# Kernel tuning notes

Measured on AMD Instinct MI355X. Metric: run time of the kernel, lower is better.

The kernel has to match this reference:

```python
import jax, jax.numpy as jnp
import numpy as np

N = 50000      # nodes
E = 800000     # edges (before self loops)
IN = 256       # in_dim
HID = 64       # hidden_dim
H = 4          # heads
OUT = 32       # out_dim (latent); conv2 out_channels = 2*OUT
NEG_SLOPE = 0.2
EPS = 1e-5


def setup_inputs() -> dict:
    key = jax.random.key(0)
    ks = jax.random.split(key, 12)
    s = 0.05
    x = jax.random.normal(ks[0], (N, IN), dtype=jnp.float32)
    edge_index = jax.random.randint(ks[1], (2, E), 0, N, dtype=jnp.int64)
    # conv1: GATv2Conv(IN -> HID, heads=H, concat=True)
    W1l = jax.random.normal(ks[2], (IN, H * HID), dtype=jnp.float32) * s
    W1r = jax.random.normal(ks[3], (IN, H * HID), dtype=jnp.float32) * s
    att1 = jax.random.normal(ks[4], (H, HID), dtype=jnp.float32) * s
    b1 = jnp.zeros((H * HID,), dtype=jnp.float32)
    # BatchNorm1 (affine)
    g1 = jnp.ones((H * HID,), dtype=jnp.float32) + 0.1 * jax.random.normal(ks[5], (H * HID,), dtype=jnp.float32)
    be1 = 0.1 * jax.random.normal(ks[6], (H * HID,), dtype=jnp.float32)
    # conv2: GATv2Conv(H*HID -> 2*OUT, heads=H, concat=False)
    W2l = jax.random.normal(ks[7], (H * HID, H * 2 * OUT), dtype=jnp.float32) * s
    W2r = jax.random.normal(ks[8], (H * HID, H * 2 * OUT), dtype=jnp.float32) * s
    att2 = jax.random.normal(ks[9], (H, 2 * OUT), dtype=jnp.float32) * s
    b2 = jnp.zeros((2 * OUT,), dtype=jnp.float32)
    return {"x": x, "edge_index": edge_index, "W1l": W1l, "W1r": W1r,
            "att1": att1, "b1": b1, "g1": g1, "be1": be1,
            "W2l": W2l, "W2r": W2r, "att2": att2, "b2": b2}


def _gatv2(x, Wl, Wr, att, bias, src, dst, heads, ch, concat):
    # PyG GATv2Conv: xl = lin_l(x) (source side), xr = lin_r(x) (target side)
    xl = (x @ Wl).reshape(N, heads, ch)
    xr = (x @ Wr).reshape(N, heads, ch)
    e = jax.nn.leaky_relu(xl[src] + xr[dst], NEG_SLOPE)      # [E', H, C]
    score = jnp.einsum('ehc,hc->eh', e, att)                 # [E', H]
    # segment softmax over edges grouped by destination node
    m = jax.ops.segment_max(score, dst, num_segments=N)
    ex = jnp.exp(score - m[dst])
    den = jax.ops.segment_sum(ex, dst, num_segments=N)
    alpha = ex / den[dst]                                    # [E', H]
    out = jax.ops.segment_sum(alpha[..., None] * xl[src], dst, num_segments=N)  # [N, H, C]
    out = out.reshape(N, heads * ch) if concat else out.mean(axis=1)
    return out + bias


def _bn(x, gamma, beta):
    mu = x.mean(axis=0)
    var = x.var(axis=0)  # biased, as in nn.BatchNorm1d training mode
    xh = (x - mu) / jnp.sqrt(var + EPS)
    if gamma is None:
        return xh
    return xh * gamma + beta


def reference(x, edge_index, W1l, W1r, att1, b1, g1, be1, W2l, W2r, att2, b2):
    loops = jnp.arange(N, dtype=edge_index.dtype)
    src = jnp.concatenate([edge_index[0], loops])
    dst = jnp.concatenate([edge_index[1], loops])
    h = _gatv2(x, W1l, W1r, att1, b1, src, dst, H, HID, True)   # [N, H*HID]
    h = jax.nn.relu(_bn(h, g1, be1))
    o = _gatv2(h, W2l, W2r, att2, b2, src, dst, H, 2 * OUT, False)  # [N, 2*OUT]
    z_mu = _bn(o[:, :OUT], None, None)          # BatchNorm(affine=False)
    z_sig = jax.nn.sigmoid(o[:, OUT:])
    return (z_mu, z_sig)
```

## Files before the change

### kernel.cpp

```cpp
#include <hip/hip_runtime.h>
#include <math.h>

#define EPSBN 1e-5f

typedef __attribute__((ext_vector_type(8))) short short8;
typedef __attribute__((ext_vector_type(8))) _Float16 f16x8;
typedef __attribute__((ext_vector_type(2))) _Float16 h2;
typedef __attribute__((ext_vector_type(4))) float f32x4;

#if defined(__has_builtin)
#if __has_builtin(__builtin_amdgcn_fdot2)
#define HAVE_FDOT2 1
#endif
#endif

__device__ __forceinline__ unsigned short f2h(float f) {
  _Float16 h = (_Float16)f;
  return __builtin_bit_cast(unsigned short, h);
}
__device__ __forceinline__ h2 bch(unsigned u) { return __builtin_bit_cast(h2, u); }
__device__ __forceinline__ unsigned h2u(h2 v) { return __builtin_bit_cast(unsigned, v); }
__device__ __forceinline__ int swz(int b) { return b ^ (((b >> 7) & 3) << 4); }

__global__ __launch_bounds__(256) void gemm_dual(const unsigned short* __restrict__ Ab,
                                                 const unsigned short* __restrict__ Wt,
                                                 unsigned short* __restrict__ C, int M) {
  __shared__ __align__(16) short As[4096];
  __shared__ __align__(16) short Bs[4096];
  const int tid = threadIdx.x;
  const int lane = tid & 63, w = tid >> 6;
  const int wr = w >> 1, wc = w & 1;
  const int bm = blockIdx.x * 128, bn = blockIdx.y * 128;

  const int srow = tid >> 2;
  const int scol = (tid & 3) << 4;
  const char* gA = (const char*)Ab + (size_t)(bm + srow) * 512 + scol;
  const char* gB = (const char*)Wt + (size_t)(bn + srow) * 512 + scol;
  char* wA0 = (char*)As + swz(tid * 16);
  char* wA1 = (char*)As + swz((256 + tid) * 16);
  char* wB0 = (char*)Bs + swz(tid * 16);
  char* wB1 = (char*)Bs + swz((256 + tid) * 16);

  int aoff[4], boff[4];
#pragma unroll
  for (int i = 0; i < 4; ++i) {
    aoff[i] = swz(((wr * 64 + i * 16 + (lane & 15)) << 6) + ((lane >> 4) << 4));
    boff[i] = swz(((wc * 64 + i * 16 + (lane & 15)) << 6) + ((lane >> 4) << 4));
  }

  f32x4 acc[4][4] = {};
  short8 ra0 = *(const short8*)(gA);
  short8 ra1 = *(const short8*)(gA + 64 * 512);
  short8 rb0 = *(const short8*)(gB);
  short8 rb1 = *(const short8*)(gB + 64 * 512);

  for (int ks = 0; ks < 8; ++ks) {
    *(short8*)wA0 = ra0; *(short8*)wA1 = ra1;
    *(short8*)wB0 = rb0; *(short8*)wB1 = rb1;
    __syncthreads();
    if (ks < 7) {
      int off = (ks + 1) * 64;
      ra0 = *(const short8*)(gA + off);
      ra1 = *(const short8*)(gA + 64 * 512 + off);
      rb0 = *(const short8*)(gB + off);
      rb1 = *(const short8*)(gB + 64 * 512 + off);
    }
    short8 af[4], bfr[4];
#pragma unroll
    for (int i = 0; i < 4; ++i) af[i] = *(const short8*)((const char*)As + aoff[i]);
#pragma unroll
    for (int i = 0; i < 4; ++i) bfr[i] = *(const short8*)((const char*)Bs + boff[i]);
#pragma unroll
    for (int mr = 0; mr < 4; ++mr)
#pragma unroll
      for (int nc = 0; nc < 4; ++nc)
        acc[mr][nc] = __builtin_amdgcn_mfma_f32_16x16x32_f16(
            __builtin_bit_cast(f16x8, bfr[nc]), __builtin_bit_cast(f16x8, af[mr]),
            acc[mr][nc], 0, 0, 0);
    __syncthreads();
  }

#pragma unroll
  for (int mr = 0; mr < 4; ++mr) {
    int row = bm + wr * 64 + mr * 16 + (lane & 15);
    if (row < M) {
#pragma unroll
      for (int nc = 0; nc < 4; ++nc) {
        int col = bn + wc * 64 + nc * 16 + ((lane >> 4) << 2);
        ushort4 o;
        o.x = f2h(acc[mr][nc][0]); o.y = f2h(acc[mr][nc][1]);
        o.z = f2h(acc[mr][nc][2]); o.w = f2h(acc[mr][nc][3]);
        *(ushort4*)&C[(size_t)row * 512 + col] = o;
      }
    }
  }
}

__global__ void prep(const float* __restrict__ x, const float* __restrict__ W1l,
                     const float* __restrict__ W1r, const float* __restrict__ W2l,
                     const float* __restrict__ W2r, const int* __restrict__ ei,
                     unsigned short* __restrict__ xh, unsigned short* __restrict__ Wt1,
                     unsigned short* __restrict__ Wt2, int* __restrict__ cnt,
                     int n4x, int Etot, int E) {
  int t = blockIdx.x * 256 + threadIdx.x;
  if (t < n4x) {
    float4 v = *(const float4*)&x[(size_t)t * 4];
    ushort4 o;
    o.x = f2h(v.x); o.y = f2h(v.y); o.z = f2h(v.z); o.w = f2h(v.w);
    *(ushort4*)&xh[(size_t)t * 4] = o;
    return;
  }
  t -= n4x;
  if (t < 131072) {
    int n = t >> 8, k = t & 255;
    const float* W = (n < 256) ? W1l : W1r;
    Wt1[t] = f2h(W[k * 256 + (n & 255)]);
    return;
  }
  t -= 131072;
  if (t < 131072) {
    int n = t >> 8, k = t & 255;
    const float* W = (n < 256) ? W2l : W2r;
    Wt2[t] = f2h(W[k * 256 + (n & 255)]);
    return;
  }
  t -= 131072;
  if (t < Etot) {
    int d = (t < E) ? ei[E + t] : t - E;
    atomicAdd(&cnt[d], 1);
  }
}

__global__ __launch_bounds__(1024) void scan_block(const int* __restrict__ cnt,
                                                   int* __restrict__ rowptr,
                                                   int N, int Etot) {
  __shared__ int lds[1024];
  int t = threadIdx.x;
  int strip = (N + 1023) >> 10;
  int lo = t * strip, hi = min(lo + strip, N);
  int s = 0;
  for (int i = lo; i < hi && lo < N; ++i) s += cnt[i];
  lds[t] = s;
  __syncthreads();
  for (int off = 1; off < 1024; off <<= 1) {
    int v = (t >= off) ? lds[t - off] : 0;
    __syncthreads();
    lds[t] += v;
    __syncthreads();
  }
  int base = lds[t] - s;
  for (int i = lo; i < hi && lo < N; ++i) { rowptr[i] = base; base += cnt[i]; }
  if (t == 1023) rowptr[N] = Etot;
}

__global__ void scatter_src(const int* __restrict__ ei, const int* __restrict__ rowptr,
                            int* __restrict__ cur, int* __restrict__ srcs,
                            int Etot, int E) {
  int e = blockIdx.x * 256 + threadIdx.x;
  if (e >= Etot) return;
  int s, d;
  if (e < E) { s = ei[e]; d = ei[E + e]; } else { s = e - E; d = s; }
  int pos = rowptr[d] + atomicAdd(&cur[d], 1);
  srcs[pos] = s;
}

template <int CONCAT>
__global__ __launch_bounds__(256) void gat_fused(const unsigned short* __restrict__ xlr,
                                                 const float* __restrict__ att,
                                                 const float* __restrict__ bias,
                                                 const int* __restrict__ rowptr,
                                                 const int* __restrict__ srcs,
                                                 void* __restrict__ outv, int N) {
  int d = (blockIdx.x << 2) + (threadIdx.x >> 6);
  if (d >= N) return;
  int lane = threadIdx.x & 63;
  uint2 ub = *(const uint2*)&xlr[(size_t)d * 512 + 256 + lane * 4];
  h2 xb01 = bch(ub.x), xb23 = bch(ub.y);
  float4 wf = *(const float4*)&att[lane * 4];
  h2 w06a = {(_Float16)(0.6f * wf.x), (_Float16)(0.6f * wf.y)};
  h2 w06b = {(_Float16)(0.6f * wf.z), (_Float16)(0.6f * wf.w)};
  h2 w04a = {(_Float16)(0.4f * wf.x), (_Float16)(0.4f * wf.y)};
  h2 w04b = {(_Float16)(0.4f * wf.z), (_Float16)(0.4f * wf.w)};
  int i0 = rowptr[d], end = rowptr[d + 1];
  int eM1 = end - 1;
  float den = 0.f, a0 = 0.f, a1 = 0.f, a2 = 0.f, a3 = 0.f;

  auto GLD = [&](int j) -> uint2 {
    int jj = min(j, eM1);
    return *(const uint2*)&xlr[(size_t)srcs[jj] * 512 + lane * 4];
  };
  auto PROC = [&](uint2 cur) {
    h2 c01 = bch(cur.x), c23 = bch(cur.y);
    h2 e01 = c01 + xb01, e23 = c23 + xb23;
    float p;
#ifdef HAVE_FDOT2
    h2 ab01 = bch(h2u(e01) & 0x7FFF7FFFu);
    h2 ab23 = bch(h2u(e23) & 0x7FFF7FFFu);
    p = __builtin_amdgcn_fdot2(ab01, w04a,
        __builtin_amdgcn_fdot2(ab23, w04b,
        __builtin_amdgcn_fdot2(e01, w06a,
        __builtin_amdgcn_fdot2(e23, w06b, 0.f, false), false), false), false);
#else
    {
      float e0 = (float)e01.x, e1 = (float)e01.y, e2 = (float)e23.x, e3 = (float)e23.y;
      float l0 = fmaxf(e0, 0.2f * e0), l1 = fmaxf(e1, 0.2f * e1);
      float l2 = fmaxf(e2, 0.2f * e2), l3 = fmaxf(e3, 0.2f * e3);
      p = l0 * wf.x + l1 * wf.y + l2 * wf.z + l3 * wf.w;
    }
#endif
    p += __shfl_xor(p, 1);
    p += __shfl_xor(p, 2);
    p += __shfl_xor(p, 4);
    p += __shfl_xor(p, 8);
    float ex = __expf(p);
    den += ex;
    a0 = fmaf(ex, (float)c01.x, a0);
    a1 = fmaf(ex, (float)c01.y, a1);
    a2 = fmaf(ex, (float)c23.x, a2);
    a3 = fmaf(ex, (float)c23.y, a3);
  };

  uint2 b0 = GLD(i0), b1 = GLD(i0 + 1), b2 = GLD(i0 + 2), b3 = GLD(i0 + 3);
  for (int i = i0; i < end; i += 4) {
    uint2 c0 = b0, c1 = b1, c2 = b2, c3 = b3;
    b0 = GLD(i + 4); b1 = GLD(i + 5); b2 = GLD(i + 6); b3 = GLD(i + 7);
    PROC(c0);
    if (i + 1 < end) PROC(c1);
    if (i + 2 < end) PROC(c2);
    if (i + 3 < end) PROC(c3);
  }

  float inv = 1.f / den;
  if (CONCAT) {
    float4 bb = *(const float4*)&bias[lane * 4];
    ushort4 o;
    o.x = f2h(a0 * inv + bb.x); o.y = f2h(a1 * inv + bb.y);
    o.z = f2h(a2 * inv + bb.z); o.w = f2h(a3 * inv + bb.w);
    *(ushort4*)&((unsigned short*)outv)[(size_t)d * 256 + lane * 4] = o;
  } else {
    float v0 = a0 * inv, v1 = a1 * inv, v2 = a2 * inv, v3 = a3 * inv;
    v0 += __shfl_xor(v0, 16); v0 += __shfl_xor(v0, 32);
    v1 += __shfl_xor(v1, 16); v1 += __shfl_xor(v1, 32);
    v2 += __shfl_xor(v2, 16); v2 += __shfl_xor(v2, 32);
    v3 += __shfl_xor(v3, 16); v3 += __shfl_xor(v3, 32);
    if (lane < 16) {
      float4 bb = *(const float4*)&bias[lane * 4];
      *(float4*)&((float*)outv)[(size_t)d * 64 + lane * 4] =
          make_float4(0.25f * v0 + bb.x, 0.25f * v1 + bb.y,
                      0.25f * v2 + bb.z, 0.25f * v3 + bb.w);
    }
  }
}

__global__ __launch_bounds__(256) void bn_stats(const unsigned short* __restrict__ h,
                                                float* __restrict__ sums, int N) {
  __shared__ float4 rs[4][64], rq[4][64];
  int lane = threadIdx.x & 63;
  int rg = threadIdx.x >> 6;
  int c4 = lane * 4;
  float s0 = 0, s1 = 0, s2 = 0, s3 = 0, q0 = 0, q1 = 0, q2 = 0, q3 = 0;
  for (int r = blockIdx.x * 4 + rg; r < N; r += gridDim.x * 4) {
    uint2 v = *(const uint2*)&h[(size_t)r * 256 + c4];
    h2 a = bch(v.x), b = bch(v.y);
    float f0 = (float)a.x, f1 = (float)a.y, f2 = (float)b.x, f3 = (float)b.y;
    s0 += f0; q0 += f0 * f0;
    s1 += f1; q1 += f1 * f1;
    s2 += f2; q2 += f2 * f2;
    s3 += f3; q3 += f3 * f3;
  }
  rs[rg][lane] = make_float4(s0, s1, s2, s3);
  rq[rg][lane] = make_float4(q0, q1, q2, q3);
  __syncthreads();
  if (rg == 0) {
    float4 S = rs[0][lane], Q = rq[0][lane];
#pragma unroll
    for (int g = 1; g < 4; ++g) {
      float4 t = rs[g][lane]; S.x += t.x; S.y += t.y; S.z += t.z; S.w += t.w;
      float4 u = rq[g][lane]; Q.x += u.x; Q.y += u.y; Q.z += u.z; Q.w += u.w;
    }
    atomicAdd(&sums[c4 + 0], S.x); atomicAdd(&sums[c4 + 1], S.y);
    atomicAdd(&sums[c4 + 2], S.z); atomicAdd(&sums[c4 + 3], S.w);
    atomicAdd(&sums[256 + c4 + 0], Q.x); atomicAdd(&sums[256 + c4 + 1], Q.y);
    atomicAdd(&sums[256 + c4 + 2], Q.z); atomicAdd(&sums[256 + c4 + 3], Q.w);
  }
}

__global__ void bn_coef(const float* __restrict__ sums, const float* __restrict__ g,
                        const float* __restrict__ be, float* __restrict__ coef, int N) {
  int c = threadIdx.x;
  float inv_n = 1.f / (float)N;
  float mu = sums[c] * inv_n;
  float var = sums[256 + c] * inv_n - mu * mu;
  float sc = g[c] * rsqrtf(var + EPSBN);
  coef[c] = sc;
  coef[256 + c] = be[c] - mu * sc;
}

__global__ void bn_apply_relu(unsigned short* __restrict__ h, const float* __restrict__ coef,
                              int N) {
  int i = blockIdx.x * 256 + threadIdx.x;
  if (i >= N * 32) return;
  int base = i * 8, c = base & 255;
  uint4 v = *(const uint4*)&h[base];
  h2 p0 = bch(v.x), p1 = bch(v.y), p2 = bch(v.z), p3 = bch(v.w);
  float4 sA = *(const float4*)&coef[c];
  float4 sB = *(const float4*)&coef[c + 4];
  float4 hA = *(const float4*)&coef[256 + c];
  float4 hB = *(const float4*)&coef[256 + c + 4];
  float r0 = fmaf((float)p0.x, sA.x, hA.x); r0 = r0 > 0.f ? r0 : 0.f;
  float r1 = fmaf((float)p0.y, sA.y, hA.y); r1 = r1 > 0.f ? r1 : 0.f;
  float r2 = fmaf((float)p1.x, sA.z, hA.z); r2 = r2 > 0.f ? r2 : 0.f;
  float r3 = fmaf((float)p1.y, sA.w, hA.w); r3 = r3 > 0.f ? r3 : 0.f;
  float r4 = fmaf((float)p2.x, sB.x, hB.x); r4 = r4 > 0.f ? r4 : 0.f;
  float r5 = fmaf((float)p2.y, sB.y, hB.y); r5 = r5 > 0.f ? r5 : 0.f;
  float r6 = fmaf((float)p3.x, sB.z, hB.z); r6 = r6 > 0.f ? r6 : 0.f;
  float r7 = fmaf((float)p3.y, sB.w, hB.w); r7 = r7 > 0.f ? r7 : 0.f;
  uint4 o;
  o.x = (unsigned)f2h(r0) | ((unsigned)f2h(r1) << 16);
  o.y = (unsigned)f2h(r2) | ((unsigned)f2h(r3) << 16);
  o.z = (unsigned)f2h(r4) | ((unsigned)f2h(r5) << 16);
  o.w = (unsigned)f2h(r6) | ((unsigned)f2h(r7) << 16);
  *(uint4*)&h[base] = o;
}

__global__ __launch_bounds__(256) void bn2_stats(const float* __restrict__ o,
                                                 float* __restrict__ sums, int N) {
  __shared__ float4 lsum[256], lqum[256];
  int t = threadIdx.x;
  int q = t & 7, rs = t >> 3;
  float4 S = {0, 0, 0, 0}, Q = {0, 0, 0, 0};
  for (int r = blockIdx.x * 32 + rs; r < N; r += gridDim.x * 32) {
    float4 v = *(const float4*)&o[(size_t)r * 64 + q * 4];
    S.x += v.x; Q.x += v.x * v.x;
    S.y += v.y; Q.y += v.y * v.y;
    S.z += v.z; Q.z += v.z * v.z;
    S.w += v.w; Q.w += v.w * v.w;
  }
  lsum[t] = S; lqum[t] = Q;
  __syncthreads();
  if (t < 8) {
    float4 Sa = lsum[t], Qa = lqum[t];
    for (int k = 1; k < 32; ++k) {
      float4 a = lsum[t + 8 * k], b = lqum[t + 8 * k];
      Sa.x += a.x; Sa.y += a.y; Sa.z += a.z; Sa.w += a.w;
      Qa.x += b.x; Qa.y += b.y; Qa.z += b.z; Qa.w += b.w;
    }
    atomicAdd(&sums[t * 4 + 0], Sa.x); atomicAdd(&sums[t * 4 + 1], Sa.y);
    atomicAdd(&sums[t * 4 + 2], Sa.z); atomicAdd(&sums[t * 4 + 3], Sa.w);
    atomicAdd(&sums[32 + t * 4 + 0], Qa.x); atomicAdd(&sums[32 + t * 4 + 1], Qa.y);
    atomicAdd(&sums[32 + t * 4 + 2], Qa.z); atomicAdd(&sums[32 + t * 4 + 3], Qa.w);
  }
}

__global__ void write_out(const float* __restrict__ o, const float* __restrict__ sums,
                          float* __restrict__ out, int N) {
  int t = threadIdx.x;
  int n = blockIdx.x * 4 + (t >> 6);
  if (n >= N) return;
  int lane = t & 63;
  float v = o[(size_t)n * 64 + lane];
  if (lane < 32) {
    float inv_n = 1.f / (float)N;
    float mu = sums[lane] * inv_n;
    float var = sums[32 + lane] * inv_n - mu * mu;
    out[(size_t)n * 32 + lane] = (v - mu) * rsqrtf(var + EPSBN);
  } else {
    out[(size_t)N * 32 + (size_t)n * 32 + (lane - 32)] = 1.f / (1.f + __expf(-v));
  }
}

extern "C" void kernel_launch(void* const* d_in, const int* in_sizes, int n_in,
                              void* d_out, int out_size, void* d_ws, size_t ws_size,
                              hipStream_t stream) {
  const float* x    = (const float*)d_in[0];
  const int*   ei   = (const int*)d_in[1];
  const float* W1l  = (const float*)d_in[2];
  const float* W1r  = (const float*)d_in[3];
  const float* att1 = (const float*)d_in[4];
  const float* b1   = (const float*)d_in[5];
  const float* g1   = (const float*)d_in[6];
  const float* be1  = (const float*)d_in[7];
  const float* W2l  = (const float*)d_in[8];
  const float* W2r  = (const float*)d_in[9];
  const float* att2 = (const float*)d_in[10];
  const float* b2   = (const float*)d_in[11];
  float* out = (float*)d_out;

  const int N = in_sizes[0] / 256;
  const int E = in_sizes[1] / 2;
  const int Etot = E + N;
  const int Npad = ((N + 127) / 128) * 128;

  char* ws = (char*)d_ws;
  unsigned short* xh  = (unsigned short*)ws; ws += (size_t)Npad * 256 * 2;
  unsigned short* hb  = (unsigned short*)ws; ws += (size_t)Npad * 256 * 2;
  unsigned short* AB  = (unsigned short*)ws; ws += (size_t)Npad * 512 * 2;
  unsigned short* Wt1 = (unsigned short*)ws; ws += (size_t)512 * 256 * 2;
  unsigned short* Wt2 = (unsigned short*)ws; ws += (size_t)512 * 256 * 2;
  float* o    = (float*)ws;  ws += (size_t)N * 64 * 4;
  int* rowptr = (int*)ws;    ws += (size_t)(N + 1) * 4;
  int* cnt    = (int*)ws;    ws += (size_t)N * 4;
  int* srcs   = (int*)ws;    ws += (size_t)Etot * 4;
  float* sums1 = (float*)ws; ws += 512 * 4;
  float* sums2 = (float*)ws; ws += 64 * 4;
  float* coef1 = (float*)ws; ws += 512 * 4;

  dim3 gemmGrid(Npad / 128, 4);
  int dstBlocks = (N + 3) / 4;
  int n4x = N * 64;
  int prepTotal = n4x + 131072 + 131072 + Etot;

  hipMemsetAsync(cnt, 0, (size_t)N * 4, stream);
  hipMemsetAsync(sums1, 0, 512 * 4, stream);
  hipMemsetAsync(sums2, 0, 64 * 4, stream);
  prep<<<(prepTotal + 255) / 256, 256, 0, stream>>>(x, W1l, W1r, W2l, W2r, ei,
                                                    xh, Wt1, Wt2, cnt, n4x, Etot, E);
  scan_block<<<1, 1024, 0, stream>>>(cnt, rowptr, N, Etot);
  hipMemsetAsync(cnt, 0, (size_t)N * 4, stream);
  scatter_src<<<(Etot + 255) / 256, 256, 0, stream>>>(ei, rowptr, cnt, srcs, Etot, E);

  gemm_dual<<<gemmGrid, 256, 0, stream>>>(xh, Wt1, AB, N);
  gat_fused<1><<<dstBlocks, 256, 0, stream>>>(AB, att1, b1, rowptr, srcs, hb, N);
  bn_stats<<<512, 256, 0, stream>>>(hb, sums1, N);
  bn_coef<<<1, 256, 0, stream>>>(sums1, g1, be1, coef1, N);
  bn_apply_relu<<<(N * 32 + 255) / 256, 256, 0, stream>>>(hb, coef1, N);

  gemm_dual<<<gemmGrid, 256, 0, stream>>>(hb, Wt2, AB, N);
  gat_fused<0><<<dstBlocks, 256, 0, stream>>>(AB, att2, b2, rowptr, srcs, o, N);
  bn2_stats<<<128, 256, 0, stream>>>(o, sums2, N);
  write_out<<<dstBlocks, 256, 0, stream>>>(o, sums2, out, N);
}
```

Measured before the change: 610.4 us.

## Replace single-block CSR scan with three-phase multi-block scan

```diff
diff --git a/kernel.cpp b/kernel.cpp
--- a/kernel.cpp
+++ b/kernel.cpp
@@ -131,26 +131,76 @@
   }
 }
 
-__global__ __launch_bounds__(1024) void scan_block(const int* __restrict__ cnt,
-                                                   int* __restrict__ rowptr,
-                                                   int N, int Etot) {
-  __shared__ int lds[1024];
+__global__ __launch_bounds__(256) void scan_partial(const int* __restrict__ cnt,
+                                                    int* __restrict__ bsum, int N) {
+  __shared__ int red[256];
   int t = threadIdx.x;
-  int strip = (N + 1023) >> 10;
-  int lo = t * strip, hi = min(lo + strip, N);
+  int i = blockIdx.x * 1024 + t * 4;
   int s = 0;
-  for (int i = lo; i < hi && lo < N; ++i) s += cnt[i];
-  lds[t] = s;
+  if (i + 3 < N) {
+    int4 v = *(const int4*)&cnt[i];
+    s = v.x + v.y + v.z + v.w;
+  } else {
+    for (int k = 0; k < 4; ++k)
+      if (i + k < N) s += cnt[i + k];
+  }
+  red[t] = s;
   __syncthreads();
-  for (int off = 1; off < 1024; off <<= 1) {
-    int v = (t >= off) ? lds[t - off] : 0;
+  for (int off = 128; off > 0; off >>= 1) {
+    if (t < off) red[t] += red[t + off];
     __syncthreads();
-    lds[t] += v;
+  }
+  if (t == 0) bsum[blockIdx.x] = red[0];
+}
+
+__global__ void scan_bsums(const int* __restrict__ bsum, int* __restrict__ boff,
+                           int* __restrict__ rowptr, int nb, int N, int Etot) {
+  int t = threadIdx.x;
+  int v = (t < nb) ? bsum[t] : 0;
+  int x = v;
+  for (int off = 1; off < 64; off <<= 1) {
+    int y = __shfl_up(x, off);
+    if (t >= off) x += y;
+  }
+  if (t < nb) boff[t] = x - v;
+  if (t == 0) rowptr[N] = Etot;
+}
+
+__global__ __launch_bounds__(256) void scan_final(int* __restrict__ cnt,
+                                                  const int* __restrict__ boff,
+                                                  int* __restrict__ rowptr, int N) {
+  __shared__ int red[256];
+  int t = threadIdx.x;
+  int i = blockIdx.x * 1024 + t * 4;
+  int c0 = 0, c1 = 0, c2 = 0, c3 = 0;
+  if (i + 3 < N) {
+    int4 v = *(const int4*)&cnt[i];
+    c0 = v.x; c1 = v.y; c2 = v.z; c3 = v.w;
+    *(int4*)&cnt[i] = make_int4(0, 0, 0, 0);
+  } else {
+    if (i + 0 < N) { c0 = cnt[i + 0]; cnt[i + 0] = 0; }
+    if (i + 1 < N) { c1 = cnt[i + 1]; cnt[i + 1] = 0; }
+    if (i + 2 < N) { c2 = cnt[i + 2]; cnt[i + 2] = 0; }
+    if (i + 3 < N) { c3 = cnt[i + 3]; cnt[i + 3] = 0; }
+  }
+  int s = c0 + c1 + c2 + c3;
+  red[t] = s;
+  __syncthreads();
+  for (int off = 1; off < 256; off <<= 1) {
+    int y = (t >= off) ? red[t - off] : 0;
     __syncthreads();
-  }
-  int base = lds[t] - s;
-  for (int i = lo; i < hi && lo < N; ++i) { rowptr[i] = base; base += cnt[i]; }
-  if (t == 1023) rowptr[N] = Etot;
+    red[t] += y;
+    __syncthreads();
+  }
+  int excl = red[t] - s + boff[blockIdx.x];
+  if (i + 3 < N) {
+    *(int4*)&rowptr[i] = make_int4(excl, excl + c0, excl + c0 + c1, excl + c0 + c1 + c2);
+  } else {
+    if (i + 0 < N) rowptr[i + 0] = excl;
+    if (i + 1 < N) rowptr[i + 1] = excl + c0;
+    if (i + 2 < N) rowptr[i + 2] = excl + c0 + c1;
+    if (i + 3 < N) rowptr[i + 3] = excl + c0 + c1 + c2;
+  }
 }
 
 __global__ void scatter_src(const int* __restrict__ ei, const int* __restrict__ rowptr,
@@ -390,6 +440,7 @@
   const int E = in_sizes[1] / 2;
   const int Etot = E + N;
   const int Npad = ((N + 127) / 128) * 128;
+  const int nb = (N + 1023) / 1024;
 
   char* ws = (char*)d_ws;
   unsigned short* xh  = (unsigned short*)ws; ws += (size_t)Npad * 256 * 2;
@@ -401,6 +452,8 @@
   int* rowptr = (int*)ws;    ws += (size_t)(N + 1) * 4;
   int* cnt    = (int*)ws;    ws += (size_t)N * 4;
   int* srcs   = (int*)ws;    ws += (size_t)Etot * 4;
+  int* bsum   = (int*)ws;    ws += 64 * 4;
+  int* boff   = (int*)ws;    ws += 64 * 4;
   float* sums1 = (float*)ws; ws += 512 * 4;
   float* sums2 = (float*)ws; ws += 64 * 4;
   float* coef1 = (float*)ws; ws += 512 * 4;
@@ -415,8 +468,9 @@
   hipMemsetAsync(sums2, 0, 64 * 4, stream);
   prep<<<(prepTotal + 255) / 256, 256, 0, stream>>>(x, W1l, W1r, W2l, W2r, ei,
                                                     xh, Wt1, Wt2, cnt, n4x, Etot, E);
-  scan_block<<<1, 1024, 0, stream>>>(cnt, rowptr, N, Etot);
-  hipMemsetAsync(cnt, 0, (size_t)N * 4, stream);
+  scan_partial<<<nb, 256, 0, stream>>>(cnt, bsum, N);
+  scan_bsums<<<1, 64, 0, stream>>>(bsum, boff, rowptr, nb, N, Etot);
+  scan_final<<<nb, 256, 0, stream>>>(cnt, boff, rowptr, N);
   scatter_src<<<(Etot + 255) / 256, 256, 0, stream>>>(ei, rowptr, cnt, srcs, Etot, E);
 
   gemm_dual<<<gemmGrid, 256, 0, stream>>>(xh, Wt1, AB, N);
```

Measured after the change: 517.0 us. 15.3% less time.
